# Optimization experiments

Hardware: AMD Instinct MI355X
Metric: run time of the kernel (lower is better)

Reference implementation:

```python
import jax, jax.numpy as jnp
import numpy as np

HEADS = 8
DIM_HEAD = 64  # note: per-head dim is inner_dim/heads = 512 due to the module's inner_dim = dim_head*dim
SCALE = DIM_HEAD ** (-0.5)
EPS = 1e-5


def layernorm(x, gamma):
    # nn.LayerNorm(dim, elementwise_affine=False) then x * (gamma + 1)
    mu = jnp.mean(x, axis=-1, keepdims=True)
    var = jnp.var(x, axis=-1, keepdims=True)
    xn = (x - mu) * jax.lax.rsqrt(var + EPS)
    return xn * (gamma + 1.0)


def setup_inputs() -> dict:
    key = jax.random.key(0)
    ks = jax.random.split(key, 6)
    b, n, dim = 2, 2048, 256
    inner = DIM_HEAD * dim  # 4096
    x = jax.random.normal(ks[0], (b, n, dim), dtype=jnp.float32)
    gamma = jax.random.normal(ks[1], (dim,), dtype=jnp.float32) * 0.02
    Wq = jax.random.normal(ks[2], (inner, dim), dtype=jnp.float32) * 0.02
    Wk = jax.random.normal(ks[3], (inner, dim), dtype=jnp.float32) * 0.02
    Wv = jax.random.normal(ks[4], (inner, dim), dtype=jnp.float32) * 0.02
    Wo = jax.random.normal(ks[5], (dim, inner), dtype=jnp.float32) * 0.02
    return {"x": x, "gamma": gamma, "Wq": Wq, "Wk": Wk, "Wv": Wv, "Wo": Wo}


def reference(x, gamma, Wq, Wk, Wv, Wo):
    b, n, dim = x.shape
    h = HEADS
    xn = layernorm(x, gamma)  # reuse_attention=True -> norm = LayerNorm(dim)
    # self-attention: context = xn (cross_attend=False, norm_context=Identity)
    q = jnp.einsum('bnd,ed->bne', xn, Wq).reshape(b, n, h, -1).transpose(0, 2, 1, 3)
    k = jnp.einsum('bnd,ed->bne', xn, Wk).reshape(b, n, h, -1).transpose(0, 2, 1, 3)
    v = jnp.einsum('bnd,ed->bne', xn, Wv).reshape(b, n, h, -1).transpose(0, 2, 1, 3)
    qk_sim = jnp.einsum('bhqd,bhkd->bhqk', q * SCALE, k)
    attn = jax.nn.softmax(qk_sim, axis=-1)  # dropout p=0.0 -> identity
    dot = jnp.einsum('bhqk,bhkd->bhqd', attn, v)
    out = dot.transpose(0, 2, 1, 3).reshape(b, n, -1)
    out = jnp.einsum('bne,de->bnd', out, Wo)
    return out
```

## Files before the change

kernel.cpp:

```cpp
#include <hip/hip_runtime.h>


typedef unsigned short u16;
typedef unsigned int u32;
typedef __bf16 bf16x8 __attribute__((ext_vector_type(8)));
typedef float f32x4 __attribute__((ext_vector_type(4)));

__device__ __forceinline__ u16 f2bf(float f) {
    u32 u = __builtin_bit_cast(u32, f);
    u += 0x7fffu + ((u >> 16) & 1u);
    return (u16)(u >> 16);
}

#define GLDS16(G, L)                                                                  \
    __builtin_amdgcn_global_load_lds((const __attribute__((address_space(1))) u32*)(G), \
                                     (__attribute__((address_space(3))) u32*)(L), 16, 0, 0)

template <typename OutT, bool ATOMIC>
__global__ void __launch_bounds__(256, 4) gemm_bt(
    const u16* __restrict__ A, const u16* __restrict__ B, OutT* __restrict__ C,
    int K, int lda, int ldb, int ldc,
    long sAh, long sAb, long sBh, long sBb, long sCh, long sCb,
    int H, int NB, long ksA, long ksB)
{
    __shared__ u16 ldsA[2][128 * 32];
    __shared__ u16 ldsB[2][128 * 32];

    const int z = blockIdx.z;
    const int zh = z % H;
    const int zq = z / H;
    const int zb = zq % NB;
    const int kc = zq / NB;
    A += (size_t)zh * sAh + (size_t)zb * sAb + (size_t)kc * ksA;
    B += (size_t)zh * sBh + (size_t)zb * sBb + (size_t)kc * ksB;
    C += (size_t)zh * sCh + (size_t)zb * sCb;

    const int bm = blockIdx.y * 128;
    const int bn = blockIdx.x * 128;
    const int t = threadIdx.x;
    const int w = t >> 6, l = t & 63;
    const int wm = w >> 1, wn = w & 1;
    const int lr = l & 15, lk = l >> 4;
    const int sw = lk ^ ((lr >> 1) & 3);

    const int m0 = t >> 2, s0 = t & 3;
    const int c0 = s0 ^ ((m0 >> 1) & 3);
    const int m1 = 64 + m0;
    const int c1 = s0 ^ ((m1 >> 1) & 3);
    const int o0 = (t & ~63) * 8;
    const int o1 = (256 + (t & ~63)) * 8;

    const u16* gA0 = A + (size_t)(bm + m0) * lda + c0 * 8;
    const u16* gA1 = A + (size_t)(bm + m1) * lda + c1 * 8;
    const u16* gB0 = B + (size_t)(bn + m0) * ldb + c0 * 8;
    const u16* gB1 = B + (size_t)(bn + m1) * ldb + c1 * 8;

    f32x4 acc[4][4];
#pragma unroll
    for (int i = 0; i < 4; ++i)
#pragma unroll
        for (int j = 0; j < 4; ++j)
            acc[i][j] = f32x4{0.f, 0.f, 0.f, 0.f};

    const int nk = K >> 5;

    GLDS16(gA0, &ldsA[0][o0]); GLDS16(gA1, &ldsA[0][o1]);
    GLDS16(gB0, &ldsB[0][o0]); GLDS16(gB1, &ldsB[0][o1]);
    gA0 += 32; gA1 += 32; gB0 += 32; gB1 += 32;
    __syncthreads();

    for (int kt = 0; kt < nk; ++kt) {
        const int cb = kt & 1;
        if (kt + 1 < nk) {
            GLDS16(gA0, &ldsA[cb ^ 1][o0]); GLDS16(gA1, &ldsA[cb ^ 1][o1]);
            GLDS16(gB0, &ldsB[cb ^ 1][o0]); GLDS16(gB1, &ldsB[cb ^ 1][o1]);
            gA0 += 32; gA1 += 32; gB0 += 32; gB1 += 32;
        }
        bf16x8 av[4], bv[4];
#pragma unroll
        for (int i = 0; i < 4; ++i) {
            av[i] = *(const bf16x8*)&ldsA[cb][(wm * 64 + i * 16 + lr) * 32 + sw * 8];
            bv[i] = *(const bf16x8*)&ldsB[cb][(wn * 64 + i * 16 + lr) * 32 + sw * 8];
        }
#pragma unroll
        for (int i = 0; i < 4; ++i)
#pragma unroll
            for (int j = 0; j < 4; ++j)
                acc[i][j] = __builtin_amdgcn_mfma_f32_16x16x32_bf16(av[i], bv[j], acc[i][j], 0, 0, 0);
        if (kt + 1 < nk) __syncthreads();
    }

#pragma unroll
    for (int i = 0; i < 4; ++i) {
        const int row0 = bm + wm * 64 + i * 16 + lk * 4;
#pragma unroll
        for (int j = 0; j < 4; ++j) {
            const int col = bn + wn * 64 + j * 16 + lr;
#pragma unroll
            for (int r = 0; r < 4; ++r) {
                const size_t idx = (size_t)(row0 + r) * ldc + col;
                const float v = acc[i][j][r];
                if constexpr (ATOMIC) {
                    atomicAdd(&C[idx], v);
                } else if constexpr (sizeof(OutT) == 2) {
                    C[idx] = (OutT)f2bf(v);
                } else {
                    C[idx] = (OutT)v;
                }
            }
        }
    }
}

__global__ void __launch_bounds__(256, 2) attn_fused(
    const u16* __restrict__ Y, const u16* __restrict__ xn,
    const u16* __restrict__ Zt, float* __restrict__ out)
{
    __shared__ u16 ldsB[2][128 * 32];
    __shared__ u16 ldsZ[2][256 * 32];
    __shared__ u16 Pl[64 * 136];
    __shared__ float l_lds[64];

    const int i0 = blockIdx.x * 64;
    const int hb = blockIdx.y;
    const int h = hb >> 1, b = hb & 1;

    const int t = threadIdx.x;
    const int w = t >> 6, l = t & 63;
    const int wm = w >> 1, wn = w & 1;
    const int lr = l & 15, lk = l >> 4;
    const int sw = lk ^ ((lr >> 1) & 3);

    if (t < 64) l_lds[t] = 0.f;

    const u16* Yb = Y + (size_t)(b * 2048 + i0) * 2048 + h * 256;
    const u16* xb = xn + (size_t)b * 2048 * 256;
    const u16* Zb = Zt + (size_t)b * 4194304 + (size_t)h * 524288;

    const int m0 = t >> 2, s0 = t & 3;
    const int c0 = s0 ^ ((m0 >> 1) & 3);
    const int m1 = 64 + m0;
    const int c1 = s0 ^ ((m1 >> 1) & 3);
    const int oB0 = (t & ~63) * 8;
    const int oB1 = (256 + (t & ~63)) * 8;

    const u16 *gZ0, *gZ1, *gZ2, *gZ3;
    const int oZ0 = (t & ~63) * 8;
    const int oZ1 = (256 + (t & ~63)) * 8;
    const int oZ2 = (512 + (t & ~63)) * 8;
    const int oZ3 = (768 + (t & ~63)) * 8;
    {
        const int q0 = t, q1 = 256 + t, q2 = 512 + t, q3 = 768 + t;
        const int mz0 = q0 >> 2, mz1 = q1 >> 2, mz2 = q2 >> 2, mz3 = q3 >> 2;
        const int cz0 = (q0 & 3) ^ ((mz0 >> 1) & 3);
        const int cz1 = (q1 & 3) ^ ((mz1 >> 1) & 3);
        const int cz2 = (q2 & 3) ^ ((mz2 >> 1) & 3);
        const int cz3 = (q3 & 3) ^ ((mz3 >> 1) & 3);
        gZ0 = Zb + (size_t)mz0 * 2048 + cz0 * 8;
        gZ1 = Zb + (size_t)mz1 * 2048 + cz1 * 8;
        gZ2 = Zb + (size_t)mz2 * 2048 + cz2 * 8;
        gZ3 = Zb + (size_t)mz3 * 2048 + cz3 * 8;
    }

    u16* ldsY = &ldsZ[0][0];
#pragma unroll
    for (int p = 0; p < 8; ++p) {
        const int q = p * 256 + t;
        const int kt = q >> 8, qq = q & 255;
        const int m = qq >> 2, s = qq & 3;
        const int c = s ^ ((m >> 1) & 3);
        GLDS16(Yb + (size_t)m * 2048 + kt * 32 + c * 8,
               &ldsY[(p * 256 + (t & ~63)) * 8]);
    }
    GLDS16(xb + (size_t)m0 * 256 + c0 * 8, &ldsB[0][oB0]);
    GLDS16(xb + (size_t)m1 * 256 + c1 * 8, &ldsB[0][oB1]);
    __syncthreads();

    bf16x8 yr[8][2];
#pragma unroll
    for (int kt = 0; kt < 8; ++kt)
#pragma unroll
        for (int i = 0; i < 2; ++i)
            yr[kt][i] = *(const bf16x8*)&ldsY[kt * 2048 + (wm * 32 + i * 16 + lr) * 32 + sw * 8];

    f32x4 acc_o[2][8];
#pragma unroll
    for (int i = 0; i < 2; ++i)
#pragma unroll
        for (int j = 0; j < 8; ++j)
            acc_o[i][j] = f32x4{0.f, 0.f, 0.f, 0.f};
    float lsum[8];
#pragma unroll
    for (int i = 0; i < 8; ++i) lsum[i] = 0.f;

    for (int jt = 0; jt < 16; ++jt) {
        const int j0 = jt * 128;

        f32x4 acc_s[2][4];
#pragma unroll
        for (int i = 0; i < 2; ++i)
#pragma unroll
            for (int j = 0; j < 4; ++j)
                acc_s[i][j] = f32x4{0.f, 0.f, 0.f, 0.f};

#pragma unroll
        for (int kt = 0; kt < 8; ++kt) {
            const int cb = kt & 1;
            if (kt < 7) {
                GLDS16(xb + (size_t)(j0 + m0) * 256 + (kt + 1) * 32 + c0 * 8, &ldsB[cb ^ 1][oB0]);
                GLDS16(xb + (size_t)(j0 + m1) * 256 + (kt + 1) * 32 + c1 * 8, &ldsB[cb ^ 1][oB1]);
            } else {
                GLDS16(gZ0 + j0, &ldsZ[0][oZ0]);
                GLDS16(gZ1 + j0, &ldsZ[0][oZ1]);
                GLDS16(gZ2 + j0, &ldsZ[0][oZ2]);
                GLDS16(gZ3 + j0, &ldsZ[0][oZ3]);
            }
            bf16x8 bv[4];
#pragma unroll
            for (int j = 0; j < 4; ++j)
                bv[j] = *(const bf16x8*)&ldsB[cb][(wn * 64 + j * 16 + lr) * 32 + sw * 8];
#pragma unroll
            for (int i = 0; i < 2; ++i)
#pragma unroll
                for (int j = 0; j < 4; ++j)
                    acc_s[i][j] = __builtin_amdgcn_mfma_f32_16x16x32_bf16(yr[kt][i], bv[j], acc_s[i][j], 0, 0, 0);
            if (kt < 7) __syncthreads();
        }

#pragma unroll
        for (int i = 0; i < 2; ++i)
#pragma unroll
            for (int j = 0; j < 4; ++j)
#pragma unroll
                for (int r = 0; r < 4; ++r) {
                    const float e = __expf(acc_s[i][j][r]);
                    lsum[i * 4 + r] += e;
                    Pl[(wm * 32 + i * 16 + lk * 4 + r) * 136 + wn * 64 + j * 16 + lr] = f2bf(e);
                }
        __syncthreads();

#pragma unroll
        for (int kt = 0; kt < 4; ++kt) {
            const int cz = kt & 1;
            if (kt < 3) {
                GLDS16(gZ0 + j0 + (kt + 1) * 32, &ldsZ[cz ^ 1][oZ0]);
                GLDS16(gZ1 + j0 + (kt + 1) * 32, &ldsZ[cz ^ 1][oZ1]);
                GLDS16(gZ2 + j0 + (kt + 1) * 32, &ldsZ[cz ^ 1][oZ2]);
                GLDS16(gZ3 + j0 + (kt + 1) * 32, &ldsZ[cz ^ 1][oZ3]);
            } else if (jt < 15) {
                GLDS16(xb + (size_t)(j0 + 128 + m0) * 256 + c0 * 8, &ldsB[0][oB0]);
                GLDS16(xb + (size_t)(j0 + 128 + m1) * 256 + c1 * 8, &ldsB[0][oB1]);
            }
            bf16x8 av[2];
#pragma unroll
            for (int i = 0; i < 2; ++i)
                av[i] = *(const bf16x8*)&Pl[(wm * 32 + i * 16 + lr) * 136 + kt * 32 + lk * 8];
#pragma unroll
            for (int jf = 0; jf < 8; ++jf) {
                const bf16x8 bz = *(const bf16x8*)&ldsZ[cz][(wn * 128 + jf * 16 + lr) * 32 + sw * 8];
#pragma unroll
                for (int i = 0; i < 2; ++i)
                    acc_o[i][jf] = __builtin_amdgcn_mfma_f32_16x16x32_bf16(av[i], bz, acc_o[i][jf], 0, 0, 0);
            }
            __syncthreads();
        }
    }

#pragma unroll
    for (int i = 0; i < 2; ++i)
#pragma unroll
        for (int r = 0; r < 4; ++r) {
            float s = lsum[i * 4 + r];
            s += __shfl_xor(s, 1, 64);
            s += __shfl_xor(s, 2, 64);
            s += __shfl_xor(s, 4, 64);
            s += __shfl_xor(s, 8, 64);
            if (lr == 0) atomicAdd(&l_lds[wm * 32 + i * 16 + lk * 4 + r], s);
        }
    __syncthreads();

#pragma unroll
    for (int i = 0; i < 2; ++i)
#pragma unroll
        for (int r = 0; r < 4; ++r) {
            const int row = wm * 32 + i * 16 + lk * 4 + r;
            const float rl = 1.0f / l_lds[row];
            float* orow = out + (size_t)(b * 2048 + i0 + row) * 256 + wn * 128;
#pragma unroll
            for (int jf = 0; jf < 8; ++jf)
                atomicAdd(&orow[jf * 16 + lr], acc_o[i][jf][r] * rl);
        }
}

__global__ void __launch_bounds__(256) tcast3_kernel(const float* __restrict__ Wq,
                                                     const float* __restrict__ Wk,
                                                     const float* __restrict__ Wv,
                                                     u16* __restrict__ dst)
{
    __shared__ u16 tile[64][66];
    const int z = blockIdx.z;
    const int wsel = z >> 3, h = z & 7;
    const float* src = (wsel == 0) ? Wq : (wsel == 1) ? Wk : Wv;
    const float scale = (wsel == 0) ? 0.125f : 1.0f;
    u16* d = dst + (size_t)wsel * 4194304;
    const int d0 = blockIdx.x * 64;
    const int a0 = blockIdx.y * 64;
    const int t = threadIdx.x;
    const int c = t & 63, r0 = t >> 6;
#pragma unroll
    for (int rr = 0; rr < 16; ++rr) {
        const int r = r0 + rr * 4;
        tile[r][c] = f2bf(src[((size_t)h * 2048 + d0 + r) * 256 + a0 + c] * scale);
    }
    __syncthreads();
#pragma unroll
    for (int rr = 0; rr < 16; ++rr) {
        const int r = r0 + rr * 4;
        d[((size_t)h * 256 + a0 + r) * 2048 + d0 + c] = tile[c][r];
    }
}

__global__ void __launch_bounds__(64) ln_kernel(const float* __restrict__ x,
                                                const float* __restrict__ g,
                                                u16* __restrict__ xn)
{
    const size_t row = blockIdx.x;
    const int l = threadIdx.x;
    const float4 v = ((const float4*)(x + row * 256))[l];
    float s = v.x + v.y + v.z + v.w;
    float q = v.x * v.x + v.y * v.y + v.z * v.z + v.w * v.w;
#pragma unroll
    for (int o = 32; o > 0; o >>= 1) {
        s += __shfl_xor(s, o, 64);
        q += __shfl_xor(q, o, 64);
    }
    const float mu = s * (1.0f / 256.0f);
    const float var = q * (1.0f / 256.0f) - mu * mu;
    const float rs = rsqrtf(var + 1e-5f);
    const float4 gg = ((const float4*)g)[l];
    ushort4 o4;
    o4.x = f2bf((v.x - mu) * rs * (gg.x + 1.0f));
    o4.y = f2bf((v.y - mu) * rs * (gg.y + 1.0f));
    o4.z = f2bf((v.z - mu) * rs * (gg.z + 1.0f));
    o4.w = f2bf((v.w - mu) * rs * (gg.w + 1.0f));
    ((ushort4*)(xn + row * 256))[l] = o4;
}

__global__ void __launch_bounds__(256) cast_bf16_kernel(const float* __restrict__ src,
                                                        u16* __restrict__ dst, float scale)
{
    const size_t i = (size_t)blockIdx.x * 256 + threadIdx.x;
    const float4 v = ((const float4*)src)[i];
    ushort4 o4;
    o4.x = f2bf(v.x * scale);
    o4.y = f2bf(v.y * scale);
    o4.z = f2bf(v.z * scale);
    o4.w = f2bf(v.w * scale);
    ((ushort4*)dst)[i] = o4;
}

extern "C" void kernel_launch(void* const* d_in, const int* in_sizes, int n_in,
                              void* d_out, int out_size, void* d_ws, size_t ws_size,
                              hipStream_t stream)
{
    (void)in_sizes; (void)n_in; (void)ws_size;
    const float* x     = (const float*)d_in[0];
    const float* gamma = (const float*)d_in[1];
    const float* Wq    = (const float*)d_in[2];
    const float* Wk    = (const float*)d_in[3];
    const float* Wv    = (const float*)d_in[4];
    const float* Wo    = (const float*)d_in[5];
    float* out = (float*)d_out;

    char* ws = (char*)d_ws;
    const size_t MB = 1048576;
    u16* wqt   = (u16*)(ws);
    u16* wkt   = (u16*)(ws + 8 * MB);
    u16* wvt   = (u16*)(ws + 16 * MB);
    u16* wo    = (u16*)(ws + 24 * MB);
    u16* xn    = (u16*)(ws + 32 * MB);
    u16* Mt    = (u16*)(ws + 34 * MB);
    u16* Nb    = (u16*)(ws + 35 * MB);
    float* MtF = (float*)(ws + 36 * MB);
    float* NbF = (float*)(ws + 38 * MB);
    u16* Y     = (u16*)(ws + 44 * MB);
    u16* Zt    = (u16*)(ws + 60 * MB);

    hipMemsetAsync(d_out, 0, (size_t)out_size * sizeof(float), stream);
    hipMemsetAsync(MtF, 0, 4 * MB, stream);

    tcast3_kernel<<<dim3(32, 4, 24), 256, 0, stream>>>(Wq, Wk, Wv, wqt);
    cast_bf16_kernel<<<4096, 256, 0, stream>>>(Wo, wo, 1.0f);
    ln_kernel<<<4096, 64, 0, stream>>>(x, gamma, xn);

    gemm_bt<float, true><<<dim3(2, 2, 32), 256, 0, stream>>>(
        wkt, wqt, MtF, 512, 2048, 2048, 256,
        524288L, 0, 524288L, 0, 65536L, 0, 8, 1, 512L, 512L);

    gemm_bt<float, true><<<dim3(2, 2, 32), 256, 0, stream>>>(
        wo, wvt, NbF, 512, 16384, 2048, 256,
        2048L, 0, 524288L, 0, 65536L, 0, 8, 1, 512L, 512L);

    cast_bf16_kernel<<<1024, 256, 0, stream>>>(MtF, Mt, 1.0f);

    gemm_bt<u16, false><<<dim3(16, 32, 1), 256, 0, stream>>>(
        xn, Mt, Y, 256, 256, 256, 2048,
        0, 0, 0, 0, 0, 0, 1, 1, 0, 0);

    gemm_bt<u16, false><<<dim3(16, 16, 2), 256, 0, stream>>>(
        Nb, xn, Zt, 256, 256, 256, 2048,
        0, 0, 0, 524288L, 0, 4194304L, 1, 2, 0, 0);

    attn_fused<<<dim3(32, 16), 256, 0, stream>>>(Y, xn, Zt, out);
}
```

Before: 283.2 us.

## Triple-buffer GEMM and attention loads with explicit vmcnt waits and XCD-aware block mapping

Both kernels move from double to triple buffering of LDS tiles. Full __syncthreads is replaced by explicit s_waitcnt vmcnt plus s_barrier, so global-to-LDS loads can stay in flight across iterations. MFMA sections are wrapped in s_setprio, and the attention kernel's workgroup IDs are remapped so each XCD handles a contiguous set of head/batch pairs for L2 locality. The extra LDS buffer lowers GEMM occupancy (launch bounds 4 to 3), and the hand-counted vmcnt values risk races if they are wrong.

```diff
diff --git a/kernel.cpp b/kernel.cpp
--- a/kernel.cpp
+++ b/kernel.cpp
@@ -16,15 +16,26 @@
     __builtin_amdgcn_global_load_lds((const __attribute__((address_space(1))) u32*)(G), \
                                      (__attribute__((address_space(3))) u32*)(L), 16, 0, 0)
 
+template <int N> __device__ __forceinline__ void vm_wait() {
+    asm volatile("s_waitcnt vmcnt(%0)" :: "n"(N) : "memory");
+}
+__device__ __forceinline__ void lgk0() {
+    asm volatile("s_waitcnt lgkmcnt(0)" ::: "memory");
+}
+__device__ __forceinline__ void bar() {
+    __builtin_amdgcn_s_barrier();
+    __builtin_amdgcn_sched_barrier(0);
+}
+
 template <typename OutT, bool ATOMIC>
-__global__ void __launch_bounds__(256, 4) gemm_bt(
+__global__ void __launch_bounds__(256, 3) gemm_bt(
     const u16* __restrict__ A, const u16* __restrict__ B, OutT* __restrict__ C,
     int K, int lda, int ldb, int ldc,
     long sAh, long sAb, long sBh, long sBb, long sCh, long sCb,
     int H, int NB, long ksA, long ksB)
 {
-    __shared__ u16 ldsA[2][128 * 32];
-    __shared__ u16 ldsB[2][128 * 32];
+    __shared__ u16 ldsA[3][128 * 32];
+    __shared__ u16 ldsB[3][128 * 32];
 
     const int z = blockIdx.z;
     const int zh = z % H;
@@ -67,27 +78,49 @@
     GLDS16(gA0, &ldsA[0][o0]); GLDS16(gA1, &ldsA[0][o1]);
     GLDS16(gB0, &ldsB[0][o0]); GLDS16(gB1, &ldsB[0][o1]);
     gA0 += 32; gA1 += 32; gB0 += 32; gB1 += 32;
-    __syncthreads();
-
-    for (int kt = 0; kt < nk; ++kt) {
-        const int cb = kt & 1;
-        if (kt + 1 < nk) {
-            GLDS16(gA0, &ldsA[cb ^ 1][o0]); GLDS16(gA1, &ldsA[cb ^ 1][o1]);
-            GLDS16(gB0, &ldsB[cb ^ 1][o0]); GLDS16(gB1, &ldsB[cb ^ 1][o1]);
+    GLDS16(gA0, &ldsA[1][o0]); GLDS16(gA1, &ldsA[1][o1]);
+    GLDS16(gB0, &ldsB[1][o0]); GLDS16(gB1, &ldsB[1][o1]);
+    gA0 += 32; gA1 += 32; gB0 += 32; gB1 += 32;
+
+    int cur = 0, wsl = 2;
+    for (int kt = 0; kt < nk - 1; ++kt) {
+        vm_wait<4>(); bar();
+        if (kt + 2 < nk) {
+            GLDS16(gA0, &ldsA[wsl][o0]); GLDS16(gA1, &ldsA[wsl][o1]);
+            GLDS16(gB0, &ldsB[wsl][o0]); GLDS16(gB1, &ldsB[wsl][o1]);
             gA0 += 32; gA1 += 32; gB0 += 32; gB1 += 32;
         }
         bf16x8 av[4], bv[4];
 #pragma unroll
         for (int i = 0; i < 4; ++i) {
-            av[i] = *(const bf16x8*)&ldsA[cb][(wm * 64 + i * 16 + lr) * 32 + sw * 8];
-            bv[i] = *(const bf16x8*)&ldsB[cb][(wn * 64 + i * 16 + lr) * 32 + sw * 8];
-        }
+            av[i] = *(const bf16x8*)&ldsA[cur][(wm * 64 + i * 16 + lr) * 32 + sw * 8];
+            bv[i] = *(const bf16x8*)&ldsB[cur][(wn * 64 + i * 16 + lr) * 32 + sw * 8];
+        }
+        __builtin_amdgcn_s_setprio(1);
 #pragma unroll
         for (int i = 0; i < 4; ++i)
 #pragma unroll
             for (int j = 0; j < 4; ++j)
                 acc[i][j] = __builtin_amdgcn_mfma_f32_16x16x32_bf16(av[i], bv[j], acc[i][j], 0, 0, 0);
-        if (kt + 1 < nk) __syncthreads();
+        __builtin_amdgcn_s_setprio(0);
+        cur = (cur == 2) ? 0 : cur + 1;
+        wsl = (wsl == 2) ? 0 : wsl + 1;
+    }
+    vm_wait<0>(); bar();
+    {
+        bf16x8 av[4], bv[4];
+#pragma unroll
+        for (int i = 0; i < 4; ++i) {
+            av[i] = *(const bf16x8*)&ldsA[cur][(wm * 64 + i * 16 + lr) * 32 + sw * 8];
+            bv[i] = *(const bf16x8*)&ldsB[cur][(wn * 64 + i * 16 + lr) * 32 + sw * 8];
+        }
+        __builtin_amdgcn_s_setprio(1);
+#pragma unroll
+        for (int i = 0; i < 4; ++i)
+#pragma unroll
+            for (int j = 0; j < 4; ++j)
+                acc[i][j] = __builtin_amdgcn_mfma_f32_16x16x32_bf16(av[i], bv[j], acc[i][j], 0, 0, 0);
+        __builtin_amdgcn_s_setprio(0);
     }
 
 #pragma unroll
@@ -116,13 +149,16 @@
     const u16* __restrict__ Y, const u16* __restrict__ xn,
     const u16* __restrict__ Zt, float* __restrict__ out)
 {
-    __shared__ u16 ldsB[2][128 * 32];
+    __shared__ u16 ldsB[3][128 * 32];
     __shared__ u16 ldsZ[2][256 * 32];
     __shared__ u16 Pl[64 * 136];
     __shared__ float l_lds[64];
 
-    const int i0 = blockIdx.x * 64;
-    const int hb = blockIdx.y;
+    const int wgid = blockIdx.x + 32 * blockIdx.y;
+    const int xcd = wgid & 7;
+    const int p = wgid >> 3;
+    const int hb = 2 * xcd + (p & 1);
+    const int i0 = (p >> 1) * 64;
     const int h = hb >> 1, b = hb & 1;
 
     const int t = threadIdx.x;
@@ -164,17 +200,20 @@
 
     u16* ldsY = &ldsZ[0][0];
 #pragma unroll
-    for (int p = 0; p < 8; ++p) {
-        const int q = p * 256 + t;
+    for (int pp = 0; pp < 8; ++pp) {
+        const int q = pp * 256 + t;
         const int kt = q >> 8, qq = q & 255;
         const int m = qq >> 2, s = qq & 3;
         const int c = s ^ ((m >> 1) & 3);
         GLDS16(Yb + (size_t)m * 2048 + kt * 32 + c * 8,
-               &ldsY[(p * 256 + (t & ~63)) * 8]);
+               &ldsY[(pp * 256 + (t & ~63)) * 8]);
     }
     GLDS16(xb + (size_t)m0 * 256 + c0 * 8, &ldsB[0][oB0]);
     GLDS16(xb + (size_t)m1 * 256 + c1 * 8, &ldsB[0][oB1]);
-    __syncthreads();
+    GLDS16(xb + (size_t)m0 * 256 + 32 + c0 * 8, &ldsB[1][oB0]);
+    GLDS16(xb + (size_t)m1 * 256 + 32 + c1 * 8, &ldsB[1][oB1]);
+    vm_wait<4>();
+    bar();
 
     bf16x8 yr[8][2];
 #pragma unroll
@@ -193,8 +232,55 @@
 #pragma unroll
     for (int i = 0; i < 8; ++i) lsum[i] = 0.f;
 
+#define S_STEP(KT, VMC, ISSUE)                                                        \
+    {                                                                                 \
+        vm_wait<VMC>(); bar();                                                        \
+        ISSUE;                                                                        \
+        bf16x8 bv[4];                                                                 \
+        _Pragma("unroll")                                                             \
+        for (int j = 0; j < 4; ++j)                                                   \
+            bv[j] = *(const bf16x8*)&ldsB[(KT) % 3][(wn * 64 + j * 16 + lr) * 32 + sw * 8]; \
+        __builtin_amdgcn_s_setprio(1);                                                \
+        _Pragma("unroll")                                                             \
+        for (int j = 0; j < 4; ++j) {                                                 \
+            acc_s[0][j] = __builtin_amdgcn_mfma_f32_16x16x32_bf16(yr[KT][0], bv[j], acc_s[0][j], 0, 0, 0); \
+            acc_s[1][j] = __builtin_amdgcn_mfma_f32_16x16x32_bf16(yr[KT][1], bv[j], acc_s[1][j], 0, 0, 0); \
+        }                                                                             \
+        __builtin_amdgcn_s_setprio(0);                                                \
+    }
+
+#define PV_STEP(KT, VMC, ISSUE)                                                       \
+    {                                                                                 \
+        vm_wait<VMC>(); bar();                                                        \
+        ISSUE;                                                                        \
+        bf16x8 av[2];                                                                 \
+        av[0] = *(const bf16x8*)&Pl[(wm * 32 + lr) * 136 + (KT) * 32 + lk * 8];       \
+        av[1] = *(const bf16x8*)&Pl[(wm * 32 + 16 + lr) * 136 + (KT) * 32 + lk * 8];  \
+        __builtin_amdgcn_s_setprio(1);                                                \
+        _Pragma("unroll")                                                             \
+        for (int jf = 0; jf < 8; ++jf) {                                              \
+            const bf16x8 bz = *(const bf16x8*)&ldsZ[(KT) & 1][(wn * 128 + jf * 16 + lr) * 32 + sw * 8]; \
+            acc_o[0][jf] = __builtin_amdgcn_mfma_f32_16x16x32_bf16(av[0], bz, acc_o[0][jf], 0, 0, 0);   \
+            acc_o[1][jf] = __builtin_amdgcn_mfma_f32_16x16x32_bf16(av[1], bz, acc_o[1][jf], 0, 0, 0);   \
+        }                                                                             \
+        __builtin_amdgcn_s_setprio(0);                                                \
+    }
+
+#define ISSUE_B(JBASE, KK, SLOT)                                                      \
+    GLDS16(JBASE + (size_t)m0 * 256 + (KK) * 32 + c0 * 8, &ldsB[SLOT][oB0]);          \
+    GLDS16(JBASE + (size_t)m1 * 256 + (KK) * 32 + c1 * 8, &ldsB[SLOT][oB1])
+
+#define ISSUE_Z(OFF, ZBUF)                                                            \
+    GLDS16(gZ0 + (OFF), &ldsZ[ZBUF][oZ0]);                                            \
+    GLDS16(gZ1 + (OFF), &ldsZ[ZBUF][oZ1]);                                            \
+    GLDS16(gZ2 + (OFF), &ldsZ[ZBUF][oZ2]);                                            \
+    GLDS16(gZ3 + (OFF), &ldsZ[ZBUF][oZ3])
+
     for (int jt = 0; jt < 16; ++jt) {
         const int j0 = jt * 128;
+        const int jn = ((jt + 1) & 15) * 128;
+        const u16* xbj = xb + (size_t)j0 * 256;
+        const u16* xbn = xb + (size_t)jn * 256;
 
         f32x4 acc_s[2][4];
 #pragma unroll
@@ -203,29 +289,14 @@
             for (int j = 0; j < 4; ++j)
                 acc_s[i][j] = f32x4{0.f, 0.f, 0.f, 0.f};
 
-#pragma unroll
-        for (int kt = 0; kt < 8; ++kt) {
-            const int cb = kt & 1;
-            if (kt < 7) {
-                GLDS16(xb + (size_t)(j0 + m0) * 256 + (kt + 1) * 32 + c0 * 8, &ldsB[cb ^ 1][oB0]);
-                GLDS16(xb + (size_t)(j0 + m1) * 256 + (kt + 1) * 32 + c1 * 8, &ldsB[cb ^ 1][oB1]);
-            } else {
-                GLDS16(gZ0 + j0, &ldsZ[0][oZ0]);
-                GLDS16(gZ1 + j0, &ldsZ[0][oZ1]);
-                GLDS16(gZ2 + j0, &ldsZ[0][oZ2]);
-                GLDS16(gZ3 + j0, &ldsZ[0][oZ3]);
-            }
-            bf16x8 bv[4];
-#pragma unroll
-            for (int j = 0; j < 4; ++j)
-                bv[j] = *(const bf16x8*)&ldsB[cb][(wn * 64 + j * 16 + lr) * 32 + sw * 8];
-#pragma unroll
-            for (int i = 0; i < 2; ++i)
-#pragma unroll
-                for (int j = 0; j < 4; ++j)
-                    acc_s[i][j] = __builtin_amdgcn_mfma_f32_16x16x32_bf16(yr[kt][i], bv[j], acc_s[i][j], 0, 0, 0);
-            if (kt < 7) __syncthreads();
-        }
+        S_STEP(0, 2, ISSUE_B(xbj, 2, 2))
+        S_STEP(1, 2, ISSUE_B(xbj, 3, 0))
+        S_STEP(2, 2, ISSUE_B(xbj, 4, 1))
+        S_STEP(3, 2, ISSUE_B(xbj, 5, 2))
+        S_STEP(4, 2, ISSUE_B(xbj, 6, 0))
+        S_STEP(5, 2, ISSUE_B(xbj, 7, 1))
+        S_STEP(6, 2, ISSUE_Z(j0, 0))
+        S_STEP(7, 4, ISSUE_Z(j0 + 32, 1))
 
 #pragma unroll
         for (int i = 0; i < 2; ++i)
@@ -237,33 +308,12 @@
                     lsum[i * 4 + r] += e;
                     Pl[(wm * 32 + i * 16 + lk * 4 + r) * 136 + wn * 64 + j * 16 + lr] = f2bf(e);
                 }
-        __syncthreads();
-
-#pragma unroll
-        for (int kt = 0; kt < 4; ++kt) {
-            const int cz = kt & 1;
-            if (kt < 3) {
-                GLDS16(gZ0 + j0 + (kt + 1) * 32, &ldsZ[cz ^ 1][oZ0]);
-                GLDS16(gZ1 + j0 + (kt + 1) * 32, &ldsZ[cz ^ 1][oZ1]);
-                GLDS16(gZ2 + j0 + (kt + 1) * 32, &ldsZ[cz ^ 1][oZ2]);
-                GLDS16(gZ3 + j0 + (kt + 1) * 32, &ldsZ[cz ^ 1][oZ3]);
-            } else if (jt < 15) {
-                GLDS16(xb + (size_t)(j0 + 128 + m0) * 256 + c0 * 8, &ldsB[0][oB0]);
-                GLDS16(xb + (size_t)(j0 + 128 + m1) * 256 + c1 * 8, &ldsB[0][oB1]);
-            }
-            bf16x8 av[2];
-#pragma unroll
-            for (int i = 0; i < 2; ++i)
-                av[i] = *(const bf16x8*)&Pl[(wm * 32 + i * 16 + lr) * 136 + kt * 32 + lk * 8];
-#pragma unroll
-            for (int jf = 0; jf < 8; ++jf) {
-                const bf16x8 bz = *(const bf16x8*)&ldsZ[cz][(wn * 128 + jf * 16 + lr) * 32 + sw * 8];
-#pragma unroll
-                for (int i = 0; i < 2; ++i)
-                    acc_o[i][jf] = __builtin_amdgcn_mfma_f32_16x16x32_bf16(av[i], bz, acc_o[i][jf], 0, 0, 0);
-            }
-            __syncthreads();
-        }
+        lgk0();
+
+        PV_STEP(0, 4, ((void)0))
+        PV_STEP(1, 0, ISSUE_Z(j0 + 64, 0))
+        PV_STEP(2, 0, ISSUE_Z(j0 + 96, 1); ISSUE_B(xbn, 0, 0))
+        PV_STEP(3, 2, ISSUE_B(xbn, 1, 1))
     }
 
 #pragma unroll
```

Result: no change. 287.1 us (+1.4%).
